# Kernel optimization log

Measured on AMD Instinct MI355X. Metric: run time of the kernel, lower is better.

## Reference

```python
import jax, jax.numpy as jnp
import numpy as np

N_BITS = 8  # total bit-width of the slice method [1,1,2,2,2]


def _quantize(t, bits=N_BITS):
    """Symmetric per-tensor fixed-point quantize->dequantize.

    This is the ideal recombination of SlicedData bit slices: the engine's
    MapReduceDot computes per-slice partial dot products and reduces them
    with powers-of-two weights, which (absent analog noise) is exactly a
    dot product of the fixed-point-quantized operands.
    """
    qmax = 2.0 ** (bits - 1) - 1.0
    scale = jnp.maximum(jnp.max(jnp.abs(t)) / qmax, 1e-12)
    return jnp.round(t / scale) * scale


def setup_inputs() -> dict:
    key = jax.random.key(0)
    k1, k2 = jax.random.split(key)
    B, D, N = 1024, 512, 16384
    x = jax.random.normal(k1, (B, D), dtype=jnp.float32)
    weight = jax.random.normal(k2, (D, N), dtype=jnp.float32)  # one vector per column
    return {"x": x, "weight": weight, "split_square_len": 32}


def reference(x, weight, split_square_len):
    B, D = x.shape
    N = weight.shape[1]
    L = split_square_len
    # bias = sum(y^2) / L, replicated L rows and stacked below the weight
    bias = jnp.sum(weight * weight, axis=0) / L            # [N]
    bias_rows = jnp.broadcast_to(bias, (L, N))             # [L, N]
    temp = jnp.concatenate([weight, bias_rows], axis=0)    # [D+L, N]
    # input padded with ones so the bias rows accumulate to sum(y^2)
    x_pad = jnp.concatenate([x, jnp.ones((B, L), dtype=x.dtype)], axis=1)  # [B, D+L]
    # MapReduceDot: bit-sliced fixed-point dot product (ideal recombination)
    out = jnp.dot(_quantize(x_pad), _quantize(temp))       # [B, N] = x@W + ||y||^2
    return out
```

## Files before the change

kernel.cpp:

```cpp
#include <hip/hip_runtime.h>
#include <hip/hip_bf16.h>

#define B_DIM 1024
#define D_DIM 512
#define N_DIM 16384

typedef __attribute__((ext_vector_type(8))) short bf16x8;
typedef __attribute__((ext_vector_type(4))) float f32x4;

#define IDX_XPART 16
#define IDX_WPART 256
#define OFF_BIAS  4096
#define OFF_XQ    69632
#define OFF_WQT   1118208

#define XMAX_BLOCKS 128
#define WSTAT_BLOCKS 256
#define QX_BLOCKS 512

__device__ inline void gload16(const void* g, void* l) {
  __builtin_amdgcn_global_load_lds((const __attribute__((address_space(1))) void*)g,
                                   (__attribute__((address_space(3))) void*)l, 16, 0, 0);
}

__device__ inline unsigned short f2bf(float f) {
  return (unsigned short)(__float_as_uint(f) >> 16);
}

__device__ inline void compute_scales(const float* __restrict__ ws_f, int lane,
                                      float& sx, float& st, float& s, float& q1) {
  float xm = fmaxf(ws_f[IDX_XPART + lane], ws_f[IDX_XPART + 64 + lane]);
  float wm = fmaxf(fmaxf(ws_f[IDX_WPART + lane], ws_f[IDX_WPART + 64 + lane]),
                   fmaxf(ws_f[IDX_WPART + 128 + lane], ws_f[IDX_WPART + 192 + lane]));
  #pragma unroll
  for (int i = 1; i < 64; i <<= 1) {
    xm = fmaxf(xm, __shfl_xor(xm, i, 64));
    wm = fmaxf(wm, __shfl_xor(wm, i, 64));
  }
  st = fmaxf(wm / 127.0f, 1e-12f);
  sx = fmaxf(fmaxf(xm, 1.0f) / 127.0f, 1e-12f);
  s = sx * st;
  q1 = rintf(1.0f / sx);
}

__global__ __launch_bounds__(256) void k_stats(const float* __restrict__ x,
                                               const float* __restrict__ w,
                                               float* __restrict__ ws_f) {
  const int t = threadIdx.x;
  if (blockIdx.x < XMAX_BLOCKS) {
    __shared__ float red[256];
    float m = 0.f;
    const float4* x4 = (const float4*)x;
    const int n4 = B_DIM * D_DIM / 4;
    for (int i = blockIdx.x * 256 + t; i < n4; i += XMAX_BLOCKS * 256) {
      float4 v = x4[i];
      m = fmaxf(m, fmaxf(fmaxf(fabsf(v.x), fabsf(v.y)), fmaxf(fabsf(v.z), fabsf(v.w))));
    }
    red[t] = m; __syncthreads();
    for (int s = 128; s > 0; s >>= 1) { if (t < s) red[t] = fmaxf(red[t], red[t + s]); __syncthreads(); }
    if (t == 0) ws_f[IDX_XPART + blockIdx.x] = red[0];
  } else {
    __shared__ float sred[256], mred[256];
    const int b = blockIdx.x - XMAX_BLOCKS;
    const int c = t & 63, part = t >> 6;
    const int col = b * 64 + c;
    float ss = 0.f, mx = 0.f;
    const float* p = w + (size_t)part * 128 * N_DIM + col;
    #pragma unroll 8
    for (int d = 0; d < 128; ++d) {
      float v = p[(size_t)d * N_DIM];
      ss += v * v;
      mx = fmaxf(mx, fabsf(v));
    }
    sred[t] = ss; mred[t] = mx;
    __syncthreads();
    if (t < 64) {
      float bsum = (sred[t] + sred[t + 64] + sred[t + 128] + sred[t + 192]) * (1.0f / 32.0f);
      ws_f[OFF_BIAS / 4 + col] = bsum;
      mred[t] = fmaxf(mred[t], bsum);
    }
    __syncthreads();
    for (int s = 128; s > 0; s >>= 1) { if (t < s) mred[t] = fmaxf(mred[t], mred[t + s]); __syncthreads(); }
    if (t == 0) ws_f[IDX_WPART + b] = mred[0];
  }
}

__global__ __launch_bounds__(256) void k_quant(const float* __restrict__ x,
                                               const float* __restrict__ w,
                                               const float* __restrict__ ws_f,
                                               unsigned short* __restrict__ xq,
                                               unsigned short* __restrict__ wqT) {
  const int t = threadIdx.x;
  float sx, st, s_u, q1_u;
  compute_scales(ws_f, t & 63, sx, st, s_u, q1_u);
  if (blockIdx.x < QX_BLOCKS) {
    const int i = blockIdx.x * 256 + t;
    float4 v = ((const float4*)x)[i];
    ushort4 o;
    o.x = f2bf(rintf(v.x / sx));
    o.y = f2bf(rintf(v.y / sx));
    o.z = f2bf(rintf(v.z / sx));
    o.w = f2bf(rintf(v.w / sx));
    ((ushort4*)xq)[i] = o;
  } else {
    __shared__ float tile[64][65];
    const int bid = blockIdx.x - QX_BLOCKS;
    const int n0 = (bid & 255) * 64, k0 = (bid >> 8) * 64;
    {
      const int tx = t & 63, ty = t >> 6;
      #pragma unroll
      for (int i = 0; i < 16; ++i) {
        int r = i * 4 + ty;
        tile[r][tx] = w[(size_t)(k0 + r) * N_DIM + n0 + tx];
      }
    }
    __syncthreads();
    const int kg = t & 15, nr = t >> 4;
    #pragma unroll
    for (int it = 0; it < 4; ++it) {
      const int nl = it * 16 + nr;
      ushort4 o;
      o.x = f2bf(rintf(tile[kg * 4 + 0][nl] / st));
      o.y = f2bf(rintf(tile[kg * 4 + 1][nl] / st));
      o.z = f2bf(rintf(tile[kg * 4 + 2][nl] / st));
      o.w = f2bf(rintf(tile[kg * 4 + 3][nl] / st));
      *(ushort4*)&wqT[(size_t)(n0 + nl) * D_DIM + k0 + kg * 4] = o;
    }
  }
}


__device__ inline void stage8(const unsigned short* __restrict__ g, int grow0, int kbase,
                              short* ldst, int w, int lane, int issue) {
  const int r0 = w * 32 + issue * 8;
  const int rl = r0 + (lane >> 3);
  const int kc = (lane & 7) ^ (lane >> 3);
  gload16(g + (size_t)(grow0 + rl) * D_DIM + kbase + kc * 8, ldst + r0 * 64);
}

__global__ __launch_bounds__(512, 2) void k_gemm(const unsigned short* __restrict__ xq,
                                                 const unsigned short* __restrict__ wqT,
                                                 const float* __restrict__ bias,
                                                 const float* __restrict__ ws_f,
                                                 float* __restrict__ out) {
  __shared__ __align__(16) short lds[2 * 32768];
  const int t = threadIdx.x;
  const int lane = t & 63, w = t >> 6;
  const int wm = w >> 2, wn = w & 3;
  const int m0 = blockIdx.y * 256, n0 = blockIdx.x * 256;

  #pragma unroll
  for (int i = 0; i < 4; ++i) {
    stage8(xq, m0, 0, &lds[0], w, lane, i);
    stage8(wqT, n0, 0, &lds[16384], w, lane, i);
  }
  float sx_u, st, s, q1;
  compute_scales(ws_f, lane, sx_u, st, s, q1);

  f32x4 acc[8][4] = {};

  asm volatile("s_waitcnt vmcnt(0)" ::: "memory");
  __builtin_amdgcn_s_barrier();
  __builtin_amdgcn_sched_barrier(0);

  for (int T = 0; T < 8; ++T) {
    short* bufA = &lds[(T & 1) * 32768];
    short* bufB = bufA + 16384;
    short* nA = &lds[((T + 1) & 1) * 32768];
    short* nB = nA + 16384;
    bf16x8 bfr[4][2];
    #pragma unroll
    for (int q = 0; q < 4; ++q) {
      if (q == 0) {
        #pragma unroll
        for (int fn = 0; fn < 4; ++fn)
          #pragma unroll
          for (int ks = 0; ks < 2; ++ks) {
            const int row = wn * 64 + fn * 16 + (lane & 15);
            const int cp = (ks * 4 + (lane >> 4)) ^ (lane & 7);
            bfr[fn][ks] = *(const bf16x8*)&bufB[row * 64 + cp * 8];
          }
      }
      bf16x8 af[2][2];
      #pragma unroll
      for (int fm = 0; fm < 2; ++fm)
        #pragma unroll
        for (int ks = 0; ks < 2; ++ks) {
          const int row = wm * 128 + (q * 2 + fm) * 16 + (lane & 15);
          const int cp = (ks * 4 + (lane >> 4)) ^ (lane & 7);
          af[fm][ks] = *(const bf16x8*)&bufA[row * 64 + cp * 8];
        }
      if (T < 7) {
        stage8(xq, m0, (T + 1) * 64, nA, w, lane, q);
        stage8(wqT, n0, (T + 1) * 64, nB, w, lane, q);
      }
      __builtin_amdgcn_s_barrier();
      __builtin_amdgcn_s_setprio(1);
      #pragma unroll
      for (int fm = 0; fm < 2; ++fm)
        #pragma unroll
        for (int ks = 0; ks < 2; ++ks)
          #pragma unroll
          for (int fn = 0; fn < 4; ++fn)
            acc[q * 2 + fm][fn] = __builtin_amdgcn_mfma_f32_16x16x32_bf16(
                af[fm][ks], bfr[fn][ks], acc[q * 2 + fm][fn], 0, 0, 0);
      __builtin_amdgcn_s_setprio(0);
      if (q == 3) asm volatile("s_waitcnt vmcnt(0)" ::: "memory");
      __builtin_amdgcn_s_barrier();
    }
    __builtin_amdgcn_sched_barrier(0);
  }

  #pragma unroll
  for (int fn = 0; fn < 4; ++fn) {
    const int col = n0 + wn * 64 + fn * 16 + (lane & 15);
    const float ba = 32.0f * q1 * rintf(bias[col] / st);
    #pragma unroll
    for (int fm = 0; fm < 8; ++fm) {
      const int rbase = m0 + wm * 128 + fm * 16 + ((lane >> 4) * 4);
      #pragma unroll
      for (int r = 0; r < 4; ++r)
        out[(size_t)(rbase + r) * N_DIM + col] = (acc[fm][fn][r] + ba) * s;
    }
  }
}

extern "C" void kernel_launch(void* const* d_in, const int* in_sizes, int n_in,
                              void* d_out, int out_size, void* d_ws, size_t ws_size,
                              hipStream_t stream) {
  const float* x = (const float*)d_in[0];
  const float* w = (const float*)d_in[1];
  float* out = (float*)d_out;
  char* ws = (char*)d_ws;
  float* ws_f = (float*)ws;
  float* bias = (float*)(ws + OFF_BIAS);
  unsigned short* xq = (unsigned short*)(ws + OFF_XQ);
  unsigned short* wqT = (unsigned short*)(ws + OFF_WQT);

  hipLaunchKernelGGL(k_stats, dim3(XMAX_BLOCKS + WSTAT_BLOCKS), dim3(256), 0, stream, x, w, ws_f);
  hipLaunchKernelGGL(k_quant, dim3(QX_BLOCKS + 2048), dim3(256), 0, stream, x, w, ws_f, xq, wqT);
  hipLaunchKernelGGL(k_gemm, dim3(N_DIM / 256, B_DIM / 256), dim3(512), 0, stream,
                     xq, wqT, bias, ws_f, out);
}
```

Baseline: 48.19 us.

## Shrink GEMM tiles to 128x128 with triple-buffered K=32 pipeline and block swizzle

Replaces the 256x256 tile, 512-thread, double-buffered K=64 GEMM with a 128x128 tile, 256-thread kernel that triple-buffers K=32 slices and keeps two loads in flight. It also remaps the 1D block index so groups of consecutive blocks share N columns and walk M rows, aiming at L2 reuse. The goal is more resident blocks (1024 instead of 256) to fill all CUs and better overlap load latency with MFMA, at the cost of lower arithmetic intensity per tile and more barriers per unit of work.

```diff
diff --git a/kernel.cpp b/kernel.cpp
--- a/kernel.cpp
+++ b/kernel.cpp
@@ -129,85 +129,67 @@
   }
 }
 
-
-__device__ inline void stage8(const unsigned short* __restrict__ g, int grow0, int kbase,
-                              short* ldst, int w, int lane, int issue) {
-  const int r0 = w * 32 + issue * 8;
-  const int rl = r0 + (lane >> 3);
-  const int kc = (lane & 7) ^ (lane >> 3);
-  gload16(g + (size_t)(grow0 + rl) * D_DIM + kbase + kc * 8, ldst + r0 * 64);
-}
-
-__global__ __launch_bounds__(512, 2) void k_gemm(const unsigned short* __restrict__ xq,
+#define NT 16
+
+__device__ inline void stage4(const unsigned short* __restrict__ xq,
+                              const unsigned short* __restrict__ wqT,
+                              int m0, int n0, int kbase, short* buf, int w, int lane) {
+  #pragma unroll
+  for (int i = 0; i < 2; ++i) {
+    const int r0 = w * 32 + i * 16;
+    const int rl = r0 + (lane >> 2);
+    const int kc = (lane & 3) ^ ((lane >> 2) & 3);
+    gload16(xq + (size_t)(m0 + rl) * D_DIM + kbase + kc * 8, buf + r0 * 32);
+    gload16(wqT + (size_t)(n0 + rl) * D_DIM + kbase + kc * 8, buf + 4096 + r0 * 32);
+  }
+}
+
+__global__ __launch_bounds__(256, 3) void k_gemm(const unsigned short* __restrict__ xq,
                                                  const unsigned short* __restrict__ wqT,
                                                  const float* __restrict__ bias,
                                                  const float* __restrict__ ws_f,
                                                  float* __restrict__ out) {
-  __shared__ __align__(16) short lds[2 * 32768];
+  __shared__ __align__(16) short lds[3 * 8192];
   const int t = threadIdx.x;
   const int lane = t & 63, w = t >> 6;
-  const int wm = w >> 2, wn = w & 3;
-  const int m0 = blockIdx.y * 256, n0 = blockIdx.x * 256;
-
-  #pragma unroll
-  for (int i = 0; i < 4; ++i) {
-    stage8(xq, m0, 0, &lds[0], w, lane, i);
-    stage8(wqT, n0, 0, &lds[16384], w, lane, i);
-  }
+  const int wm = w >> 1, wn = w & 1;
+  const int nid = (blockIdx.x & 7) * 128 + (blockIdx.x >> 3);
+  const int m0 = (nid & 7) * 128;
+  const int n0 = (nid >> 3) * 128;
+
+  stage4(xq, wqT, m0, n0, 0, &lds[0], w, lane);
+  stage4(xq, wqT, m0, n0, 32, &lds[8192], w, lane);
   float sx_u, st, s, q1;
   compute_scales(ws_f, lane, sx_u, st, s, q1);
 
-  f32x4 acc[8][4] = {};
-
-  asm volatile("s_waitcnt vmcnt(0)" ::: "memory");
+  f32x4 acc[4][4] = {};
+
+  asm volatile("s_waitcnt vmcnt(4)" ::: "memory");
   __builtin_amdgcn_s_barrier();
   __builtin_amdgcn_sched_barrier(0);
 
-  for (int T = 0; T < 8; ++T) {
-    short* bufA = &lds[(T & 1) * 32768];
-    short* bufB = bufA + 16384;
-    short* nA = &lds[((T + 1) & 1) * 32768];
-    short* nB = nA + 16384;
-    bf16x8 bfr[4][2];
-    #pragma unroll
-    for (int q = 0; q < 4; ++q) {
-      if (q == 0) {
-        #pragma unroll
-        for (int fn = 0; fn < 4; ++fn)
-          #pragma unroll
-          for (int ks = 0; ks < 2; ++ks) {
-            const int row = wn * 64 + fn * 16 + (lane & 15);
-            const int cp = (ks * 4 + (lane >> 4)) ^ (lane & 7);
-            bfr[fn][ks] = *(const bf16x8*)&bufB[row * 64 + cp * 8];
-          }
-      }
-      bf16x8 af[2][2];
+  for (int T = 0; T < NT; ++T) {
+    short* buf = &lds[(T % 3) * 8192];
+    bf16x8 af[4], bfr[4];
+    #pragma unroll
+    for (int f = 0; f < 4; ++f) {
+      const int ra = wm * 64 + f * 16 + (lane & 15);
+      af[f] = *(const bf16x8*)&buf[ra * 32 + (((lane >> 4) ^ (ra & 3))) * 8];
+      const int rb = wn * 64 + f * 16 + (lane & 15);
+      bfr[f] = *(const bf16x8*)&buf[4096 + rb * 32 + (((lane >> 4) ^ (rb & 3))) * 8];
+    }
+    if (T + 2 < NT)
+      stage4(xq, wqT, m0, n0, (T + 2) * 32, &lds[((T + 2) % 3) * 8192], w, lane);
+    __builtin_amdgcn_s_setprio(1);
+    #pragma unroll
+    for (int fm = 0; fm < 4; ++fm)
       #pragma unroll
-      for (int fm = 0; fm < 2; ++fm)
-        #pragma unroll
-        for (int ks = 0; ks < 2; ++ks) {
-          const int row = wm * 128 + (q * 2 + fm) * 16 + (lane & 15);
-          const int cp = (ks * 4 + (lane >> 4)) ^ (lane & 7);
-          af[fm][ks] = *(const bf16x8*)&bufA[row * 64 + cp * 8];
-        }
-      if (T < 7) {
-        stage8(xq, m0, (T + 1) * 64, nA, w, lane, q);
-        stage8(wqT, n0, (T + 1) * 64, nB, w, lane, q);
-      }
-      __builtin_amdgcn_s_barrier();
-      __builtin_amdgcn_s_setprio(1);
-      #pragma unroll
-      for (int fm = 0; fm < 2; ++fm)
-        #pragma unroll
-        for (int ks = 0; ks < 2; ++ks)
-          #pragma unroll
-          for (int fn = 0; fn < 4; ++fn)
-            acc[q * 2 + fm][fn] = __builtin_amdgcn_mfma_f32_16x16x32_bf16(
-                af[fm][ks], bfr[fn][ks], acc[q * 2 + fm][fn], 0, 0, 0);
-      __builtin_amdgcn_s_setprio(0);
-      if (q == 3) asm volatile("s_waitcnt vmcnt(0)" ::: "memory");
-      __builtin_amdgcn_s_barrier();
-    }
+      for (int fn = 0; fn < 4; ++fn)
+        acc[fm][fn] = __builtin_amdgcn_mfma_f32_16x16x32_bf16(af[fm], bfr[fn], acc[fm][fn], 0, 0, 0);
+    __builtin_amdgcn_s_setprio(0);
+    if (T + 2 < NT)      asm volatile("s_waitcnt vmcnt(4)" ::: "memory");
+    else if (T + 1 < NT) asm volatile("s_waitcnt vmcnt(0)" ::: "memory");
+    if (T + 1 < NT) __builtin_amdgcn_s_barrier();
     __builtin_amdgcn_sched_barrier(0);
   }
 
@@ -216,8 +198,8 @@
     const int col = n0 + wn * 64 + fn * 16 + (lane & 15);
     const float ba = 32.0f * q1 * rintf(bias[col] / st);
     #pragma unroll
-    for (int fm = 0; fm < 8; ++fm) {
-      const int rbase = m0 + wm * 128 + fm * 16 + ((lane >> 4) * 4);
+    for (int fm = 0; fm < 4; ++fm) {
+      const int rbase = m0 + wm * 64 + fm * 16 + ((lane >> 4) * 4);
       #pragma unroll
       for (int r = 0; r < 4; ++r)
         out[(size_t)(rbase + r) * N_DIM + col] = (acc[fm][fn][r] + ba) * s;
@@ -239,6 +221,6 @@
 
   hipLaunchKernelGGL(k_stats, dim3(XMAX_BLOCKS + WSTAT_BLOCKS), dim3(256), 0, stream, x, w, ws_f);
   hipLaunchKernelGGL(k_quant, dim3(QX_BLOCKS + 2048), dim3(256), 0, stream, x, w, ws_f, xq, wqT);
-  hipLaunchKernelGGL(k_gemm, dim3(N_DIM / 256, B_DIM / 256), dim3(512), 0, stream,
+  hipLaunchKernelGGL(k_gemm, dim3((B_DIM / 128) * (N_DIM / 128)), dim3(256), 0, stream,
                      xq, wqT, bias, ws_f, out);
 }
```

Measured after the change: 46.79 us. 2.9% less time.
